# Kernel optimization log

Measured on AMD Instinct MI355X. Metric: run time of the kernel, lower is better.

Reference implementation:

```python
import jax, jax.numpy as jnp
import numpy as np
from jax import lax

H, W = 3072, 4096
BLACK = 0.0625            # black level (normalized)
KNEE_X = np.array([0.0, 0.25, 1.0], np.float32)   # decompanding curve
KNEE_Y = np.array([0.0, 0.50, 1.0], np.float32)
DEN_R, DEN_EPS = 2, 100.0         # BayerDenoise defaults
AWB_MAX_GAIN = 4.0
LTM_A, LTM_B, LTM_R, LTM_EPS = 0.7, 0.0, 8, 1e-3
GAMMA = 2.2


def _box_sum_1d(x, r, axis):
    """Sliding-window sum of width 2r+1 along `axis`, edge-truncated."""
    n = x.shape[axis]
    c = jnp.cumsum(x, axis=axis)
    hi = jnp.clip(jnp.arange(n) + r, 0, n - 1)
    lo = jnp.arange(n) - r - 1
    upper = jnp.take(c, hi, axis=axis)
    lower = jnp.take(c, jnp.clip(lo, 0, n - 1), axis=axis)
    shp = [1] * x.ndim
    shp[axis] = n
    lower = lower * (lo >= 0).astype(x.dtype).reshape(shp)
    return upper - lower


def box_mean(x, r):
    """2D box mean over last two axes, normalized by valid window counts."""
    s = _box_sum_1d(_box_sum_1d(x, r, -2), r, -1)
    cnt = _box_sum_1d(_box_sum_1d(jnp.ones_like(x), r, -2), r, -1)
    return s / cnt


def guided_self(I, r, eps):
    """Self-guided (edge-preserving) filter."""
    m = box_mean(I, r)
    var = box_mean(I * I, r) - m * m
    a = var / (var + eps)
    b = m * (1.0 - a)
    return box_mean(a, r) * I + box_mean(b, r)


def conv3x3(img, k):
    return lax.conv_general_dilated(img[None, None], k[None, None], (1, 1), 'SAME')[0, 0]


def isp_pipeline(x, ccm):
    # --- DecompandBlackLevel: piecewise-linear decompand + black level ---
    x = jnp.interp(x, jnp.asarray(KNEE_X), jnp.asarray(KNEE_Y))
    x = jnp.clip((x - BLACK) / (1.0 - BLACK), 0.0, 1.0)

    # --- BayerDenoise: guided filter on each RGGB plane ---
    p = jnp.stack([x[0::2, 0::2], x[0::2, 1::2], x[1::2, 0::2], x[1::2, 1::2]])  # [4,H/2,W/2]
    p = guided_self(p, DEN_R, DEN_EPS)

    # --- AWB: gray-world gains from plane means (lum mask [0,1] = all pixels) ---
    r_m, g_m, b_m = p[0].mean(), 0.5 * (p[1].mean() + p[2].mean()), p[3].mean()
    gr = jnp.minimum(g_m / (r_m + 1e-8), AWB_MAX_GAIN)
    gb = jnp.minimum(g_m / (b_m + 1e-8), AWB_MAX_GAIN)
    x = (jnp.zeros_like(x)
         .at[0::2, 0::2].set(jnp.clip(p[0] * gr, 0.0, 1.0))
         .at[0::2, 1::2].set(jnp.clip(p[1], 0.0, 1.0))
         .at[1::2, 0::2].set(jnp.clip(p[2], 0.0, 1.0))
         .at[1::2, 1::2].set(jnp.clip(p[3] * gb, 0.0, 1.0)))

    # --- Demosaic: bilinear on RGGB mosaic ---
    ii = (jnp.arange(H) % 2)[:, None]
    jj = (jnp.arange(W) % 2)[None, :]
    mR = ((ii == 0) & (jj == 0)).astype(x.dtype)
    mG = (ii != jj).astype(x.dtype)
    mB = ((ii == 1) & (jj == 1)).astype(x.dtype)
    k_g = jnp.array([[0, 1, 0], [1, 4, 1], [0, 1, 0]], jnp.float32) / 4.0
    k_rb = jnp.array([[1, 2, 1], [2, 4, 2], [1, 2, 1]], jnp.float32) / 4.0
    rgb = jnp.stack([conv3x3(x * mR, k_rb), conv3x3(x * mG, k_g), conv3x3(x * mB, k_rb)])  # [3,H,W]

    # --- CCM ---
    rgb = jnp.clip(jnp.einsum('ij,jhw->ihw', ccm, rgb), 0.0, 1.0)

    wl = jnp.array([0.299, 0.587, 0.114], jnp.float32)
    Y = jnp.einsum('c,chw->hw', wl, rgb)
    Ys = Y.reshape(H // 2, 2, W // 2, 2).mean(axis=(1, 3))
    base = jax.image.resize(guided_self(Ys, LTM_R, LTM_EPS), (H, W), 'bilinear')
    Ynew = LTM_A * base + LTM_B + (Y - base)       # detail_gain=1, threshold=0
    rgb = jnp.clip(rgb * (Ynew / (Y + 1e-6)), 0.0, 1.0)

    # --- Gamma ---
    rgb = jnp.clip(rgb, 1e-6, 1.0) ** (1.0 / GAMMA)
    # hist_norm / post_denoise / saturation / sharpening are identity at defaults

    # --- RGBtoYUV -> NV12 (full range BT.601) ---
    R, G, B = rgb[0], rgb[1], rgb[2]
    Yf = 0.299 * R + 0.587 * G + 0.114 * B
    U = -0.168736 * R - 0.331264 * G + 0.5 * B + 0.5
    V = 0.5 * R - 0.418688 * G - 0.081312 * B + 0.5
    Us = U.reshape(H // 2, 2, W // 2, 2).mean(axis=(1, 3))
    Vs = V.reshape(H // 2, 2, W // 2, 2).mean(axis=(1, 3))
    uv = jnp.stack([Us, Vs], axis=-1).reshape(H // 2, W)  # interleaved UVUV...
    out = jnp.concatenate([Yf.reshape(-1), uv.reshape(-1)]) * 255.0
    return jnp.clip(out, 0.0, 255.0)   # float NV12 codes (pre-quantization)


def setup_inputs() -> dict:
    key = jax.random.key(0)
    k1, k2 = jax.random.split(key)
    x = jax.random.uniform(k1, (H, W), dtype=jnp.float32)
    ccm = jnp.eye(3, dtype=jnp.float32) + 0.1 * jax.random.normal(k2, (3, 3), dtype=jnp.float32)
    return {"x": x, "ccm": ccm}


def reference(x, ccm):
    return isp_pipeline(x, ccm)
```

## Files before the change

kernel.cpp:

```cpp
#include <hip/hip_runtime.h>
#include <math.h>

#define IMG_H 3072
#define IMG_W 4096
#define Hh 1536
#define Wh 2048
#define S (Hh*Wh)

#define TID 32
#define TIL 16

#if __has_builtin(__builtin_amdgcn_rcpf)
#define RCP(x) __builtin_amdgcn_rcpf(x)
#else
#define RCP(x) (1.0f/(x))
#endif

__device__ __forceinline__ float clamp01(float v){ return fminf(fmaxf(v, 0.0f), 1.0f); }

__device__ __forceinline__ float decompand_black(float v){
  float y = (v <= 0.25f) ? (2.0f*v) : fmaf(v - 0.25f, 0.5f/0.75f, 0.5f);
  y = clamp01(y);
  return clamp01((y - 0.0625f) * (1.0f/0.9375f));
}

__device__ __forceinline__ float gamma22(float x){
  return __builtin_amdgcn_exp2f(0.45454545454545453f * __builtin_amdgcn_logf(x));
}

__global__ __launch_bounds__(256) void k_split(const float* __restrict__ x, float* __restrict__ P){
  int idx = blockIdx.x*256 + threadIdx.x;
  int i = idx >> 11, j = idx & 2047;
  const float* r0 = x + (2*i)*IMG_W + 2*j;
  const float* r1 = r0 + IMG_W;
  float2 a = *(const float2*)r0;
  float2 b = *(const float2*)r1;
  P[idx]       = decompand_black(a.x);
  P[S + idx]   = decompand_black(a.y);
  P[2*S + idx] = decompand_black(b.x);
  P[3*S + idx] = decompand_black(b.y);
}

template<int TI, bool FAST>
__device__ __forceinline__ void denoise_col(const float* __restrict__ in, float* __restrict__ D,
                                            int j, int i0, float& local){
  const float inv25 = 1.0f/25.0f;
  float cw_a[5], amask[5], cw_o = 25.f;
  if (!FAST){
    #pragma unroll
    for (int k=0;k<5;++k){
      int pc = j + k - 2;
      bool ok = ((unsigned)pc < (unsigned)Wh);
      amask[k] = ok ? 1.f : 0.f;
      cw_a[k]  = ok ? (float)(min(pc+2, Wh-1) - max(pc-2, 0) + 1) : 1.f;
    }
    cw_o = (float)(min(j+2, Wh-1) - max(j-2, 0) + 1);
  }

  float rh1[5][5]={{0}}, rh2[5][5]={{0}};
  float vs1[5]={0}, vs2[5]={0};
  float rha[5]={0}, rhb[5]={0};
  float cI[5]={0};
  float wa=0.f, wb=0.f;

  const float* rp = in + (size_t)(i0-4)*Wh + j;
  float* wp = D + (size_t)i0*Wh + j;

  #pragma unroll 4
  for (int rr=0; rr<TI+8; ++rr){
    int r = i0 - 4 + rr;
    float v[9];
    if (FAST){
      #pragma unroll
      for (int d=0; d<9; ++d) v[d] = rp[d-4];
    } else {
      if ((unsigned)r < (unsigned)Hh){
        #pragma unroll
        for (int d=0; d<9; ++d){
          int c = j + d - 4;
          v[d] = ((unsigned)c < (unsigned)Wh) ? rp[d-4] : 0.f;
        }
      } else {
        #pragma unroll
        for (int d=0; d<9; ++d) v[d]=0.f;
      }
    }
    rp += Wh;
    float sq[9];
    #pragma unroll
    for (int d=0; d<9; ++d) sq[d]=v[d]*v[d];
    float h1[5], h2[5];
    h1[0]=v[0]+v[1]+v[2]+v[3]+v[4];
    h2[0]=sq[0]+sq[1]+sq[2]+sq[3]+sq[4];
    #pragma unroll
    for (int k=1;k<5;++k){
      h1[k]=h1[k-1]-v[k-1]+v[k+4];
      h2[k]=h2[k-1]-sq[k-1]+sq[k+4];
    }
    #pragma unroll
    for (int k=0;k<5;++k){
      vs1[k]+=h1[k]-rh1[k][0];
      vs2[k]+=h2[k]-rh2[k][0];
      #pragma unroll
      for (int t=0;t<4;++t){ rh1[k][t]=rh1[k][t+1]; rh2[k][t]=rh2[k][t+1]; }
      rh1[k][4]=h1[k]; rh2[k][4]=h2[k];
    }
    #pragma unroll
    for (int t=0;t<4;++t) cI[t]=cI[t+1];
    cI[4]=v[4];

    if (rr >= 4){
      int q = r-2;
      float ha_=0.f, hb_=0.f;
      if (FAST){
        #pragma unroll
        for (int k=0;k<5;++k){
          float m   = vs1[k]*inv25;
          float var = fmaf(-m, m, vs2[k]*inv25);
          float a   = var*RCP(var + 100.0f);
          float b   = fmaf(-m, a, m);
          ha_ += a; hb_ += b;
        }
      } else {
        float rmask = ((unsigned)q < (unsigned)Hh) ? 1.f : 0.f;
        float rh = (float)(min(q+2, Hh-1) - max(q-2, 0) + 1);
        #pragma unroll
        for (int k=0;k<5;++k){
          float inv = RCP(rh*cw_a[k]);
          float m   = vs1[k]*inv;
          float var = fmaf(-m, m, vs2[k]*inv);
          float a   = var*RCP(var + 100.0f);
          float b   = fmaf(-m, a, m);
          ha_ = fmaf(a, amask[k], ha_);
          hb_ = fmaf(b, amask[k], hb_);
        }
        ha_ *= rmask; hb_ *= rmask;
      }
      wa += ha_ - rha[0];
      wb += hb_ - rhb[0];
      #pragma unroll
      for (int t=0;t<4;++t){ rha[t]=rha[t+1]; rhb[t]=rhb[t+1]; }
      rha[4]=ha_; rhb[4]=hb_;

      if (rr >= 8){
        int ro = r-4;
        float invo;
        if (FAST){
          invo = inv25;
        } else {
          float rho = (float)(min(ro+2, Hh-1) - max(ro-2, 0) + 1);
          invo = RCP(rho*cw_o);
        }
        float d = fmaf(wa*invo, cI[0], wb*invo);
        *wp = d; wp += Wh;
        local += d;
      }
    }
  }
}

template<int TI>
__global__ __launch_bounds__(256) void k_denoise(const float* __restrict__ P4,
                                                 float* __restrict__ D4,
                                                 float* __restrict__ sums){
  const int j  = blockIdx.x*256 + threadIdx.x;
  const int i0 = blockIdx.y*TI;
  const int pl = blockIdx.z;
  const float* __restrict__ in = P4 + (size_t)pl*S;
  float* __restrict__ D = D4 + (size_t)pl*S;
  float local = 0.f;

  const bool fast = (blockIdx.x >= 1) && (blockIdx.x <= (Wh/256)-2) &&
                    (blockIdx.y >= 1) && (i0 + TI + 4 <= Hh);
  if (fast) denoise_col<TI, true >(in, D, j, i0, local);
  else      denoise_col<TI, false>(in, D, j, i0, local);

  __shared__ float red[256];
  red[threadIdx.x]=local;
  __syncthreads();
  #pragma unroll
  for (int off=128; off>0; off>>=1){
    if (threadIdx.x<off) red[threadIdx.x]+=red[threadIdx.x+off];
    __syncthreads();
  }
  if (threadIdx.x==0) atomicAdd(sums+pl, red[0]);
}

template<int R, int TI>
__global__ __launch_bounds__(256) void k_boxsq_ab(const float* __restrict__ in,
                                                  float* __restrict__ A, float* __restrict__ B,
                                                  float eps){
  int j  = blockIdx.x*256 + threadIdx.x;
  int i0 = blockIdx.y*TI;
  int cw = min(j+R, Wh-1) - max(j-R, 0) + 1;

  float hs[2*R+1], hs2[2*R+1];
  float ws = 0.f, ws2 = 0.f;
  #pragma unroll
  for (int k=0; k<2*R+1; ++k){
    int r = i0 - R + k;
    float s = 0.f, s2 = 0.f;
    if ((unsigned)r < (unsigned)Hh){
      const float* row = in + r*Wh;
      #pragma unroll
      for (int d=-R; d<=R; ++d){
        int c = j + d;
        float v = ((unsigned)c < (unsigned)Wh) ? row[c] : 0.f;
        s += v; s2 = fmaf(v, v, s2);
      }
    }
    hs[k] = s; hs2[k] = s2; ws += s; ws2 += s2;
  }
  #pragma unroll
  for (int t=0; t<TI; ++t){
    int i = i0 + t;
    int rh = min(i+R, Hh-1) - max(i-R, 0) + 1;
    float inv = 1.0f/(float)(rh*cw);
    float m   = ws*inv;
    float var = fmaf(-m, m, ws2*inv);
    float a   = var/(var + eps);
    A[i*Wh + j] = a;
    B[i*Wh + j] = m*(1.0f - a);
    if (t < TI-1){
      ws -= hs[0]; ws2 -= hs2[0];
      #pragma unroll
      for (int k=0; k<2*R; ++k){ hs[k]=hs[k+1]; hs2[k]=hs2[k+1]; }
      int r = i + R + 1;
      float s = 0.f, s2 = 0.f;
      if (r < Hh){
        const float* row = in + r*Wh;
        #pragma unroll
        for (int d=-R; d<=R; ++d){
          int c = j + d;
          float v = ((unsigned)c < (unsigned)Wh) ? row[c] : 0.f;
          s += v; s2 = fmaf(v, v, s2);
        }
      }
      hs[2*R] = s; hs2[2*R] = s2; ws += s; ws2 += s2;
    }
  }
}

template<int R, int TI>
__global__ __launch_bounds__(256) void k_box_apply(const float* __restrict__ in,
                                                   const float* __restrict__ A, const float* __restrict__ B,
                                                   float* __restrict__ D){
  int j  = blockIdx.x*256 + threadIdx.x;
  int i0 = blockIdx.y*TI;
  int cw = min(j+R, Wh-1) - max(j-R, 0) + 1;

  float ha[2*R+1], hb[2*R+1];
  float wa = 0.f, wb = 0.f;
  #pragma unroll
  for (int k=0; k<2*R+1; ++k){
    int r = i0 - R + k;
    float sa = 0.f, sb = 0.f;
    if ((unsigned)r < (unsigned)Hh){
      const float* ra = A + r*Wh;
      const float* rb = B + r*Wh;
      #pragma unroll
      for (int d=-R; d<=R; ++d){
        int c = j + d;
        bool ok = ((unsigned)c < (unsigned)Wh);
        sa += ok ? ra[c] : 0.f;
        sb += ok ? rb[c] : 0.f;
      }
    }
    ha[k] = sa; hb[k] = sb; wa += sa; wb += sb;
  }
  #pragma unroll
  for (int t=0; t<TI; ++t){
    int i = i0 + t;
    int rh = min(i+R, Hh-1) - max(i-R, 0) + 1;
    float inv = 1.0f/(float)(rh*cw);
    D[i*Wh + j] = fmaf(wa*inv, in[i*Wh + j], wb*inv);
    if (t < TI-1){
      wa -= ha[0]; wb -= hb[0];
      #pragma unroll
      for (int k=0; k<2*R; ++k){ ha[k]=ha[k+1]; hb[k]=hb[k+1]; }
      int r = i + R + 1;
      float sa = 0.f, sb = 0.f;
      if (r < Hh){
        const float* ra = A + r*Wh;
        const float* rb = B + r*Wh;
        #pragma unroll
        for (int d2=-R; d2<=R; ++d2){
          int c = j + d2;
          bool ok = ((unsigned)c < (unsigned)Wh);
          sa += ok ? ra[c] : 0.f;
          sb += ok ? rb[c] : 0.f;
        }
      }
      ha[2*R] = sa; hb[2*R] = sb; wa += sa; wb += sb;
    }
  }
}

__global__ void k_gains(const float* __restrict__ sums, float* __restrict__ gains){
  if (threadIdx.x == 0 && blockIdx.x == 0){
    const float inv = 1.0f/(float)S;
    float rm = sums[0]*inv, g1 = sums[1]*inv, g2 = sums[2]*inv, bm = sums[3]*inv;
    float gm = 0.5f*(g1+g2);
    gains[0] = fminf(gm/(rm + 1e-8f), 4.0f);
    gains[1] = fminf(gm/(bm + 1e-8f), 4.0f);
  }
}

__device__ __forceinline__ void load_mosaic(const float* __restrict__ D, float gr, float gb,
                                            int i, int j, float m[4][4]){
  const float* __restrict__ P0 = D;
  const float* __restrict__ P1 = D + (size_t)S;
  const float* __restrict__ P2 = D + (size_t)2*S;
  const float* __restrict__ P3 = D + (size_t)3*S;
  const bool up = (i > 0), dn = (i < Hh-1), lf = (j > 0), rt = (j < Wh-1);
  const size_t rc = (size_t)i*Wh + j;
  const size_t ru = rc - Wh, rd = rc + Wh;
  m[0][0] = (up && lf) ? clamp01(P3[ru-1]*gb) : 0.f;
  m[0][1] = up ? clamp01(P2[ru]) : 0.f;
  m[0][2] = up ? clamp01(P3[ru]*gb) : 0.f;
  m[0][3] = (up && rt) ? clamp01(P2[ru+1]) : 0.f;
  m[1][0] = lf ? clamp01(P1[rc-1]) : 0.f;
  m[1][1] = clamp01(P0[rc]*gr);
  m[1][2] = clamp01(P1[rc]);
  m[1][3] = rt ? clamp01(P0[rc+1]*gr) : 0.f;
  m[2][0] = lf ? clamp01(P3[rc-1]*gb) : 0.f;
  m[2][1] = clamp01(P2[rc]);
  m[2][2] = clamp01(P3[rc]*gb);
  m[2][3] = rt ? clamp01(P2[rc+1]) : 0.f;
  m[3][0] = (dn && lf) ? clamp01(P1[rd-1]) : 0.f;
  m[3][1] = dn ? clamp01(P0[rd]*gr) : 0.f;
  m[3][2] = dn ? clamp01(P1[rd]) : 0.f;
  m[3][3] = (dn && rt) ? clamp01(P0[rd+1]*gr) : 0.f;
}

__device__ __forceinline__ void demosaic_ccm(const float m[4][4], const float* __restrict__ C,
                                             float R[2][2], float G[2][2], float Bv[2][2]){
  float r[2][2], g[2][2], b[2][2];
  r[0][0] = m[1][1];
  g[0][0] = 0.25f*(m[0][1]+m[2][1]+m[1][0]+m[1][2]);
  b[0][0] = 0.25f*(m[0][0]+m[0][2]+m[2][0]+m[2][2]);
  r[0][1] = 0.5f*(m[1][1]+m[1][3]);
  g[0][1] = m[1][2];
  b[0][1] = 0.5f*(m[0][2]+m[2][2]);
  r[1][0] = 0.5f*(m[1][1]+m[3][1]);
  g[1][0] = m[2][1];
  b[1][0] = 0.5f*(m[2][0]+m[2][2]);
  r[1][1] = 0.25f*(m[1][1]+m[1][3]+m[3][1]+m[3][3]);
  g[1][1] = 0.25f*(m[1][2]+m[3][2]+m[2][1]+m[2][3]);
  b[1][1] = m[2][2];
  #pragma unroll
  for (int a=0; a<2; ++a){
    #pragma unroll
    for (int c=0; c<2; ++c){
      R[a][c]  = clamp01(fmaf(C[2], b[a][c], fmaf(C[1], g[a][c], C[0]*r[a][c])));
      G[a][c]  = clamp01(fmaf(C[5], b[a][c], fmaf(C[4], g[a][c], C[3]*r[a][c])));
      Bv[a][c] = clamp01(fmaf(C[8], b[a][c], fmaf(C[7], g[a][c], C[6]*r[a][c])));
    }
  }
}

__global__ __launch_bounds__(256) void k_ys(const float* __restrict__ D, const float* __restrict__ gains,
                                            const float* __restrict__ C, float* __restrict__ Ys){
  int idx = blockIdx.x*256 + threadIdx.x;
  int i = idx >> 11, j = idx & 2047;
  float gr = gains[0], gb = gains[1];
  float m[4][4]; load_mosaic(D, gr, gb, i, j, m);
  float R[2][2], G[2][2], Bv[2][2];
  demosaic_ccm(m, C, R, G, Bv);
  float y = 0.f;
  #pragma unroll
  for (int a=0; a<2; ++a)
    #pragma unroll
    for (int c=0; c<2; ++c)
      y += 0.299f*R[a][c] + 0.587f*G[a][c] + 0.114f*Bv[a][c];
  Ys[idx] = 0.25f*y;
}

__global__ __launch_bounds__(256) void k_final(const float* __restrict__ D, const float* __restrict__ gains,
                                               const float* __restrict__ C,
                                               const float* __restrict__ bs, float* __restrict__ out){
  int idx = blockIdx.x*256 + threadIdx.x;
  int i = idx >> 11, j = idx & 2047;
  float gr = gains[0], gb = gains[1];
  float m[4][4]; load_mosaic(D, gr, gb, i, j, m);
  float R[2][2], G[2][2], Bv[2][2];
  demosaic_ccm(m, C, R, G, Bv);

  float bsv[3][3];
  #pragma unroll
  for (int a=0; a<3; ++a){
    int r = min(max(i-1+a, 0), Hh-1);
    #pragma unroll
    for (int b=0; b<3; ++b){
      int c = min(max(j-1+b, 0), Wh-1);
      bsv[a][b] = bs[(r<<11) + c];
    }
  }
  float base[2][2];
  base[0][0] = 0.0625f*bsv[0][0] + 0.1875f*bsv[0][1] + 0.1875f*bsv[1][0] + 0.5625f*bsv[1][1];
  base[0][1] = 0.1875f*bsv[0][1] + 0.0625f*bsv[0][2] + 0.5625f*bsv[1][1] + 0.1875f*bsv[1][2];
  base[1][0] = 0.1875f*bsv[1][0] + 0.5625f*bsv[1][1] + 0.0625f*bsv[2][0] + 0.1875f*bsv[2][1];
  base[1][1] = 0.5625f*bsv[1][1] + 0.1875f*bsv[1][2] + 0.1875f*bsv[2][1] + 0.0625f*bsv[2][2];

  float Yp[2][2];
  float Uacc = 0.f, Vacc = 0.f;
  #pragma unroll
  for (int a=0; a<2; ++a){
    #pragma unroll
    for (int c=0; c<2; ++c){
      float Yl   = 0.299f*R[a][c] + 0.587f*G[a][c] + 0.114f*Bv[a][c];
      float Ynew = fmaf(0.7f, base[a][c], Yl - base[a][c]);
      float sc   = Ynew/(Yl + 1e-6f);
      float Rg = gamma22(fmaxf(clamp01(R[a][c]*sc),  1e-6f));
      float Gg = gamma22(fmaxf(clamp01(G[a][c]*sc),  1e-6f));
      float Bg = gamma22(fmaxf(clamp01(Bv[a][c]*sc), 1e-6f));
      float Yf = 0.299f*Rg + 0.587f*Gg + 0.114f*Bg;
      Yp[a][c] = fminf(fmaxf(Yf*255.0f, 0.0f), 255.0f);
      Uacc += -0.168736f*Rg - 0.331264f*Gg + 0.5f*Bg + 0.5f;
      Vacc +=  0.5f*Rg - 0.418688f*Gg - 0.081312f*Bg + 0.5f;
    }
  }
  *(float2*)(out + (2*i)*IMG_W   + 2*j) = make_float2(Yp[0][0], Yp[0][1]);
  *(float2*)(out + (2*i+1)*IMG_W + 2*j) = make_float2(Yp[1][0], Yp[1][1]);
  float u = fminf(fmaxf(0.25f*Uacc*255.0f, 0.0f), 255.0f);
  float v = fminf(fmaxf(0.25f*Vacc*255.0f, 0.0f), 255.0f);
  *(float2*)(out + IMG_H*IMG_W + i*IMG_W + 2*j) = make_float2(u, v);
}

extern "C" void kernel_launch(void* const* d_in, const int* in_sizes, int n_in,
                              void* d_out, int out_size, void* d_ws, size_t ws_size,
                              hipStream_t stream){
  const float* x   = (const float*)d_in[0];
  const float* ccm = (const float*)d_in[1];
  float* ws  = (float*)d_ws;
  float* out = (float*)d_out;

  size_t need = ((size_t)10*S + 8)*sizeof(float);
  if (ws_size < need) return;

  float* P  = ws;
  float* D  = ws + (size_t)4*S;
  float* Ys = ws + (size_t)8*S;
  float* La = ws + (size_t)9*S;
  float* Lb = ws;
  float* bs = ws + (size_t)S;
  float* sums  = ws + (size_t)10*S;
  float* gains = sums + 4;

  const int nb = S/256;
  dim3 gdn(Wh/256, Hh/TID, 4);
  dim3 gltm(Wh/256, Hh/TIL);

  k_split<<<nb, 256, 0, stream>>>(x, P);
  (void)hipMemsetAsync(sums, 0, 4*sizeof(float), stream);
  k_denoise<TID><<<gdn, 256, 0, stream>>>(P, D, sums);
  k_gains<<<1, 64, 0, stream>>>(sums, gains);
  k_ys<<<nb, 256, 0, stream>>>(D, gains, ccm, Ys);
  k_boxsq_ab<8, TIL><<<gltm, 256, 0, stream>>>(Ys, La, Lb, 1e-3f);
  k_box_apply<8, TIL><<<gltm, 256, 0, stream>>>(Ys, La, Lb, bs);
  k_final<<<nb, 256, 0, stream>>>(D, gains, ccm, bs, out);
}
```

Baseline: 329.8 us.

## Process two columns per thread in split, denoise, ys and final kernels

Each thread now handles two adjacent half-res columns, so horizontal box sums and neighbor loads are shared between outputs, and loads and stores are vectorized as float2 and float4. The memset and the separate gains kernel are dropped: sums are zeroed inside k_split and gains are computed inline from sums in consumers. The aim is fewer memory transactions and fewer launches, at the cost of higher register pressure in denoise and half as many threads.

```diff
diff --git a/kernel.cpp b/kernel.cpp
--- a/kernel.cpp
+++ b/kernel.cpp
@@ -28,77 +28,85 @@
   return __builtin_amdgcn_exp2f(0.45454545454545453f * __builtin_amdgcn_logf(x));
 }
 
-__global__ __launch_bounds__(256) void k_split(const float* __restrict__ x, float* __restrict__ P){
+__global__ __launch_bounds__(256) void k_split(const float* __restrict__ x, float* __restrict__ P,
+                                               float* __restrict__ sums){
   int idx = blockIdx.x*256 + threadIdx.x;
-  int i = idx >> 11, j = idx & 2047;
-  const float* r0 = x + (2*i)*IMG_W + 2*j;
-  const float* r1 = r0 + IMG_W;
-  float2 a = *(const float2*)r0;
-  float2 b = *(const float2*)r1;
-  P[idx]       = decompand_black(a.x);
-  P[S + idx]   = decompand_black(a.y);
-  P[2*S + idx] = decompand_black(b.x);
-  P[3*S + idx] = decompand_black(b.y);
+  int i = idx >> 10, jq = (idx & 1023)*2;
+  const float* r0 = x + (size_t)(2*i)*IMG_W + 2*jq;
+  float4 a = *(const float4*)r0;
+  float4 b = *(const float4*)(r0 + IMG_W);
+  size_t o = (size_t)i*Wh + jq;
+  *(float2*)(P + o)            = make_float2(decompand_black(a.x), decompand_black(a.z));
+  *(float2*)(P + S + o)        = make_float2(decompand_black(a.y), decompand_black(a.w));
+  *(float2*)(P + 2*(size_t)S + o) = make_float2(decompand_black(b.x), decompand_black(b.z));
+  *(float2*)(P + 3*(size_t)S + o) = make_float2(decompand_black(b.y), decompand_black(b.w));
+  if (blockIdx.x == 0 && threadIdx.x < 4) sums[threadIdx.x] = 0.f;
 }
 
 template<int TI, bool FAST>
-__device__ __forceinline__ void denoise_col(const float* __restrict__ in, float* __restrict__ D,
-                                            int j, int i0, float& local){
+__device__ __forceinline__ void denoise_col2(const float* __restrict__ in, float* __restrict__ D,
+                                             int c0, int i0, float& local){
   const float inv25 = 1.0f/25.0f;
-  float cw_a[5], amask[5], cw_o = 25.f;
+  float cw_a[6], amask[6], cw_o0 = 25.f, cw_o1 = 25.f;
   if (!FAST){
     #pragma unroll
-    for (int k=0;k<5;++k){
-      int pc = j + k - 2;
+    for (int k=0;k<6;++k){
+      int pc = c0 + k - 2;
       bool ok = ((unsigned)pc < (unsigned)Wh);
       amask[k] = ok ? 1.f : 0.f;
       cw_a[k]  = ok ? (float)(min(pc+2, Wh-1) - max(pc-2, 0) + 1) : 1.f;
     }
-    cw_o = (float)(min(j+2, Wh-1) - max(j-2, 0) + 1);
-  }
-
-  float rh1[5][5]={{0}}, rh2[5][5]={{0}};
-  float vs1[5]={0}, vs2[5]={0};
-  float rha[5]={0}, rhb[5]={0};
-  float cI[5]={0};
-  float wa=0.f, wb=0.f;
-
-  const float* rp = in + (size_t)(i0-4)*Wh + j;
-  float* wp = D + (size_t)i0*Wh + j;
+    cw_o0 = (float)(min(c0+2, Wh-1)   - max(c0-2, 0) + 1);
+    cw_o1 = (float)(min(c0+3, Wh-1)   - max(c0-1, 0) + 1);
+  }
+
+  float rh1[6][5]={{0}}, rh2[6][5]={{0}};
+  float vs1[6]={0}, vs2[6]={0};
+  float rha0[5]={0}, rhb0[5]={0}, rha1[5]={0}, rhb1[5]={0};
+  float cI0[5]={0}, cI1[5]={0};
+  float wa0=0.f, wb0=0.f, wa1=0.f, wb1=0.f;
+
+  const float* rp = in + (size_t)(i0-4)*Wh + c0;
+  float* wp = D + (size_t)i0*Wh + c0;
 
   #pragma unroll 4
   for (int rr=0; rr<TI+8; ++rr){
     int r = i0 - 4 + rr;
-    float v[9];
+    float v[10];
     if (FAST){
-      #pragma unroll
-      for (int d=0; d<9; ++d) v[d] = rp[d-4];
+      float2 p0 = *(const float2*)(rp-4);
+      float2 p1 = *(const float2*)(rp-2);
+      float2 p2 = *(const float2*)(rp);
+      float2 p3 = *(const float2*)(rp+2);
+      float2 p4 = *(const float2*)(rp+4);
+      v[0]=p0.x; v[1]=p0.y; v[2]=p1.x; v[3]=p1.y; v[4]=p2.x;
+      v[5]=p2.y; v[6]=p3.x; v[7]=p3.y; v[8]=p4.x; v[9]=p4.y;
     } else {
       if ((unsigned)r < (unsigned)Hh){
         #pragma unroll
-        for (int d=0; d<9; ++d){
-          int c = j + d - 4;
+        for (int d=0; d<10; ++d){
+          int c = c0 + d - 4;
           v[d] = ((unsigned)c < (unsigned)Wh) ? rp[d-4] : 0.f;
         }
       } else {
         #pragma unroll
-        for (int d=0; d<9; ++d) v[d]=0.f;
+        for (int d=0; d<10; ++d) v[d]=0.f;
       }
     }
     rp += Wh;
-    float sq[9];
-    #pragma unroll
-    for (int d=0; d<9; ++d) sq[d]=v[d]*v[d];
-    float h1[5], h2[5];
+    float sq[10];
+    #pragma unroll
+    for (int d=0; d<10; ++d) sq[d]=v[d]*v[d];
+    float h1[6], h2[6];
     h1[0]=v[0]+v[1]+v[2]+v[3]+v[4];
     h2[0]=sq[0]+sq[1]+sq[2]+sq[3]+sq[4];
     #pragma unroll
-    for (int k=1;k<5;++k){
+    for (int k=1;k<6;++k){
       h1[k]=h1[k-1]-v[k-1]+v[k+4];
       h2[k]=h2[k-1]-sq[k-1]+sq[k+4];
     }
     #pragma unroll
-    for (int k=0;k<5;++k){
+    for (int k=0;k<6;++k){
       vs1[k]+=h1[k]-rh1[k][0];
       vs2[k]+=h2[k]-rh2[k][0];
       #pragma unroll
@@ -106,54 +114,58 @@
       rh1[k][4]=h1[k]; rh2[k][4]=h2[k];
     }
     #pragma unroll
-    for (int t=0;t<4;++t) cI[t]=cI[t+1];
-    cI[4]=v[4];
+    for (int t=0;t<4;++t){ cI0[t]=cI0[t+1]; cI1[t]=cI1[t+1]; }
+    cI0[4]=v[4]; cI1[4]=v[5];
 
     if (rr >= 4){
       int q = r-2;
-      float ha_=0.f, hb_=0.f;
+      float a6[6], b6[6];
       if (FAST){
         #pragma unroll
-        for (int k=0;k<5;++k){
+        for (int k=0;k<6;++k){
           float m   = vs1[k]*inv25;
           float var = fmaf(-m, m, vs2[k]*inv25);
           float a   = var*RCP(var + 100.0f);
-          float b   = fmaf(-m, a, m);
-          ha_ += a; hb_ += b;
+          a6[k] = a; b6[k] = fmaf(-m, a, m);
         }
       } else {
         float rmask = ((unsigned)q < (unsigned)Hh) ? 1.f : 0.f;
         float rh = (float)(min(q+2, Hh-1) - max(q-2, 0) + 1);
         #pragma unroll
-        for (int k=0;k<5;++k){
+        for (int k=0;k<6;++k){
           float inv = RCP(rh*cw_a[k]);
           float m   = vs1[k]*inv;
           float var = fmaf(-m, m, vs2[k]*inv);
           float a   = var*RCP(var + 100.0f);
           float b   = fmaf(-m, a, m);
-          ha_ = fmaf(a, amask[k], ha_);
-          hb_ = fmaf(b, amask[k], hb_);
+          a6[k] = a*amask[k]*rmask; b6[k] = b*amask[k]*rmask;
         }
-        ha_ *= rmask; hb_ *= rmask;
-      }
-      wa += ha_ - rha[0];
-      wb += hb_ - rhb[0];
-      #pragma unroll
-      for (int t=0;t<4;++t){ rha[t]=rha[t+1]; rhb[t]=rhb[t+1]; }
-      rha[4]=ha_; rhb[4]=hb_;
+      }
+      float ha0 = a6[0]+a6[1]+a6[2]+a6[3]+a6[4];
+      float hb0 = b6[0]+b6[1]+b6[2]+b6[3]+b6[4];
+      float ha1 = ha0 - a6[0] + a6[5];
+      float hb1 = hb0 - b6[0] + b6[5];
+      wa0 += ha0 - rha0[0]; wb0 += hb0 - rhb0[0];
+      wa1 += ha1 - rha1[0]; wb1 += hb1 - rhb1[0];
+      #pragma unroll
+      for (int t=0;t<4;++t){
+        rha0[t]=rha0[t+1]; rhb0[t]=rhb0[t+1];
+        rha1[t]=rha1[t+1]; rhb1[t]=rhb1[t+1];
+      }
+      rha0[4]=ha0; rhb0[4]=hb0; rha1[4]=ha1; rhb1[4]=hb1;
 
       if (rr >= 8){
         int ro = r-4;
-        float invo;
-        if (FAST){
-          invo = inv25;
-        } else {
+        float invo0, invo1;
+        if (FAST){ invo0 = inv25; invo1 = inv25; }
+        else {
           float rho = (float)(min(ro+2, Hh-1) - max(ro-2, 0) + 1);
-          invo = RCP(rho*cw_o);
+          invo0 = RCP(rho*cw_o0); invo1 = RCP(rho*cw_o1);
         }
-        float d = fmaf(wa*invo, cI[0], wb*invo);
-        *wp = d; wp += Wh;
-        local += d;
+        float d0 = fmaf(wa0*invo0, cI0[0], wb0*invo0);
+        float d1 = fmaf(wa1*invo1, cI1[0], wb1*invo1);
+        *(float2*)wp = make_float2(d0, d1); wp += Wh;
+        local += d0 + d1;
       }
     }
   }
@@ -163,17 +175,18 @@
 __global__ __launch_bounds__(256) void k_denoise(const float* __restrict__ P4,
                                                  float* __restrict__ D4,
                                                  float* __restrict__ sums){
-  const int j  = blockIdx.x*256 + threadIdx.x;
+  const int c0 = (blockIdx.x*256 + threadIdx.x)*2;
   const int i0 = blockIdx.y*TI;
   const int pl = blockIdx.z;
   const float* __restrict__ in = P4 + (size_t)pl*S;
   float* __restrict__ D = D4 + (size_t)pl*S;
   float local = 0.f;
 
-  const bool fast = (blockIdx.x >= 1) && (blockIdx.x <= (Wh/256)-2) &&
-                    (blockIdx.y >= 1) && (i0 + TI + 4 <= Hh);
-  if (fast) denoise_col<TI, true >(in, D, j, i0, local);
-  else      denoise_col<TI, false>(in, D, j, i0, local);
+  const int cmin = (blockIdx.x*256 + (threadIdx.x & ~63))*2;
+  const bool rows_ok = (i0 >= 4) && (i0 + TI + 4 <= Hh);
+  const bool fast = rows_ok && (cmin >= 4) && (cmin + 131 < Wh);
+  if (fast) denoise_col2<TI, true >(in, D, c0, i0, local);
+  else      denoise_col2<TI, false>(in, D, c0, i0, local);
 
   __shared__ float red[256];
   red[threadIdx.x]=local;
@@ -296,58 +309,84 @@
   }
 }
 
-__global__ void k_gains(const float* __restrict__ sums, float* __restrict__ gains){
-  if (threadIdx.x == 0 && blockIdx.x == 0){
-    const float inv = 1.0f/(float)S;
-    float rm = sums[0]*inv, g1 = sums[1]*inv, g2 = sums[2]*inv, bm = sums[3]*inv;
-    float gm = 0.5f*(g1+g2);
-    gains[0] = fminf(gm/(rm + 1e-8f), 4.0f);
-    gains[1] = fminf(gm/(bm + 1e-8f), 4.0f);
-  }
-}
-
-__device__ __forceinline__ void load_mosaic(const float* __restrict__ D, float gr, float gb,
-                                            int i, int j, float m[4][4]){
+__device__ __forceinline__ void awb_gains(const float* __restrict__ sums, float& gr, float& gb){
+  const float invS = 1.0f/(float)S;
+  float rm = sums[0]*invS, g1 = sums[1]*invS, g2 = sums[2]*invS, bm = sums[3]*invS;
+  float gm = 0.5f*(g1+g2);
+  gr = fminf(gm/(rm + 1e-8f), 4.0f);
+  gb = fminf(gm/(bm + 1e-8f), 4.0f);
+}
+
+__device__ __forceinline__ void load_mosaic2(const float* __restrict__ D, float gr, float gb,
+                                             int i, int j, float m[4][6]){
   const float* __restrict__ P0 = D;
   const float* __restrict__ P1 = D + (size_t)S;
   const float* __restrict__ P2 = D + (size_t)2*S;
   const float* __restrict__ P3 = D + (size_t)3*S;
-  const bool up = (i > 0), dn = (i < Hh-1), lf = (j > 0), rt = (j < Wh-1);
+  const bool up = (i > 0), dn = (i < Hh-1), lf = (j > 0), rt = (j+2 < Wh);
   const size_t rc = (size_t)i*Wh + j;
   const size_t ru = rc - Wh, rd = rc + Wh;
-  m[0][0] = (up && lf) ? clamp01(P3[ru-1]*gb) : 0.f;
-  m[0][1] = up ? clamp01(P2[ru]) : 0.f;
-  m[0][2] = up ? clamp01(P3[ru]*gb) : 0.f;
-  m[0][3] = (up && rt) ? clamp01(P2[ru+1]) : 0.f;
-  m[1][0] = lf ? clamp01(P1[rc-1]) : 0.f;
-  m[1][1] = clamp01(P0[rc]*gr);
-  m[1][2] = clamp01(P1[rc]);
-  m[1][3] = rt ? clamp01(P0[rc+1]*gr) : 0.f;
-  m[2][0] = lf ? clamp01(P3[rc-1]*gb) : 0.f;
-  m[2][1] = clamp01(P2[rc]);
-  m[2][2] = clamp01(P3[rc]*gb);
-  m[2][3] = rt ? clamp01(P2[rc+1]) : 0.f;
-  m[3][0] = (dn && lf) ? clamp01(P1[rd-1]) : 0.f;
-  m[3][1] = dn ? clamp01(P0[rd]*gr) : 0.f;
-  m[3][2] = dn ? clamp01(P1[rd]) : 0.f;
-  m[3][3] = (dn && rt) ? clamp01(P0[rd+1]*gr) : 0.f;
-}
-
-__device__ __forceinline__ void demosaic_ccm(const float m[4][4], const float* __restrict__ C,
-                                             float R[2][2], float G[2][2], float Bv[2][2]){
+  const float2 z = make_float2(0.f, 0.f);
+  {
+    float2 t3 = up ? *(const float2*)(P3+ru) : z;
+    float2 t2 = up ? *(const float2*)(P2+ru) : z;
+    m[0][0] = (up&&lf) ? clamp01(P3[ru-1]*gb) : 0.f;
+    m[0][1] = clamp01(t2.x);
+    m[0][2] = clamp01(t3.x*gb);
+    m[0][3] = clamp01(t2.y);
+    m[0][4] = clamp01(t3.y*gb);
+    m[0][5] = (up&&rt) ? clamp01(P2[ru+2]) : 0.f;
+  }
+  {
+    float2 t1 = *(const float2*)(P1+rc);
+    float2 t0 = *(const float2*)(P0+rc);
+    m[1][0] = lf ? clamp01(P1[rc-1]) : 0.f;
+    m[1][1] = clamp01(t0.x*gr);
+    m[1][2] = clamp01(t1.x);
+    m[1][3] = clamp01(t0.y*gr);
+    m[1][4] = clamp01(t1.y);
+    m[1][5] = rt ? clamp01(P0[rc+2]*gr) : 0.f;
+  }
+  {
+    float2 s3 = *(const float2*)(P3+rc);
+    float2 s2 = *(const float2*)(P2+rc);
+    m[2][0] = lf ? clamp01(P3[rc-1]*gb) : 0.f;
+    m[2][1] = clamp01(s2.x);
+    m[2][2] = clamp01(s3.x*gb);
+    m[2][3] = clamp01(s2.y);
+    m[2][4] = clamp01(s3.y*gb);
+    m[2][5] = rt ? clamp01(P2[rc+2]) : 0.f;
+  }
+  {
+    float2 u1 = dn ? *(const float2*)(P1+rd) : z;
+    float2 u0 = dn ? *(const float2*)(P0+rd) : z;
+    m[3][0] = (dn&&lf) ? clamp01(P1[rd-1]) : 0.f;
+    m[3][1] = clamp01(u0.x*gr);
+    m[3][2] = clamp01(u1.x);
+    m[3][3] = clamp01(u0.y*gr);
+    m[3][4] = clamp01(u1.y);
+    m[3][5] = (dn&&rt) ? clamp01(P0[rd+2]*gr) : 0.f;
+  }
+}
+
+template<int O>
+__device__ __forceinline__ void demosaic_ccm_s(const float m[4][6], const float* __restrict__ C,
+                                               float R[2][2], float G[2][2], float Bv[2][2]){
+  #define MM(a,b) m[a][(b)+2*O]
   float r[2][2], g[2][2], b[2][2];
-  r[0][0] = m[1][1];
-  g[0][0] = 0.25f*(m[0][1]+m[2][1]+m[1][0]+m[1][2]);
-  b[0][0] = 0.25f*(m[0][0]+m[0][2]+m[2][0]+m[2][2]);
-  r[0][1] = 0.5f*(m[1][1]+m[1][3]);
-  g[0][1] = m[1][2];
-  b[0][1] = 0.5f*(m[0][2]+m[2][2]);
-  r[1][0] = 0.5f*(m[1][1]+m[3][1]);
-  g[1][0] = m[2][1];
-  b[1][0] = 0.5f*(m[2][0]+m[2][2]);
-  r[1][1] = 0.25f*(m[1][1]+m[1][3]+m[3][1]+m[3][3]);
-  g[1][1] = 0.25f*(m[1][2]+m[3][2]+m[2][1]+m[2][3]);
-  b[1][1] = m[2][2];
+  r[0][0] = MM(1,1);
+  g[0][0] = 0.25f*(MM(0,1)+MM(2,1)+MM(1,0)+MM(1,2));
+  b[0][0] = 0.25f*(MM(0,0)+MM(0,2)+MM(2,0)+MM(2,2));
+  r[0][1] = 0.5f*(MM(1,1)+MM(1,3));
+  g[0][1] = MM(1,2);
+  b[0][1] = 0.5f*(MM(0,2)+MM(2,2));
+  r[1][0] = 0.5f*(MM(1,1)+MM(3,1));
+  g[1][0] = MM(2,1);
+  b[1][0] = 0.5f*(MM(2,0)+MM(2,2));
+  r[1][1] = 0.25f*(MM(1,1)+MM(1,3)+MM(3,1)+MM(3,3));
+  g[1][1] = 0.25f*(MM(1,2)+MM(3,2)+MM(2,1)+MM(2,3));
+  b[1][1] = MM(2,2);
+  #undef MM
   #pragma unroll
   for (int a=0; a<2; ++a){
     #pragma unroll
@@ -359,72 +398,89 @@
   }
 }
 
-__global__ __launch_bounds__(256) void k_ys(const float* __restrict__ D, const float* __restrict__ gains,
+__global__ __launch_bounds__(256) void k_ys(const float* __restrict__ D, const float* __restrict__ sums,
                                             const float* __restrict__ C, float* __restrict__ Ys){
   int idx = blockIdx.x*256 + threadIdx.x;
-  int i = idx >> 11, j = idx & 2047;
-  float gr = gains[0], gb = gains[1];
-  float m[4][4]; load_mosaic(D, gr, gb, i, j, m);
-  float R[2][2], G[2][2], Bv[2][2];
-  demosaic_ccm(m, C, R, G, Bv);
-  float y = 0.f;
-  #pragma unroll
-  for (int a=0; a<2; ++a)
-    #pragma unroll
-    for (int c=0; c<2; ++c)
-      y += 0.299f*R[a][c] + 0.587f*G[a][c] + 0.114f*Bv[a][c];
-  Ys[idx] = 0.25f*y;
-}
-
-__global__ __launch_bounds__(256) void k_final(const float* __restrict__ D, const float* __restrict__ gains,
+  int i = idx >> 10, j = (idx & 1023)*2;
+  float gr, gb; awb_gains(sums, gr, gb);
+  float m[4][6]; load_mosaic2(D, gr, gb, i, j, m);
+  float y0 = 0.f, y1 = 0.f;
+  {
+    float R[2][2], G[2][2], Bv[2][2];
+    demosaic_ccm_s<0>(m, C, R, G, Bv);
+    #pragma unroll
+    for (int a=0; a<2; ++a)
+      #pragma unroll
+      for (int c=0; c<2; ++c)
+        y0 += 0.299f*R[a][c] + 0.587f*G[a][c] + 0.114f*Bv[a][c];
+  }
+  {
+    float R[2][2], G[2][2], Bv[2][2];
+    demosaic_ccm_s<1>(m, C, R, G, Bv);
+    #pragma unroll
+    for (int a=0; a<2; ++a)
+      #pragma unroll
+      for (int c=0; c<2; ++c)
+        y1 += 0.299f*R[a][c] + 0.587f*G[a][c] + 0.114f*Bv[a][c];
+  }
+  *(float2*)(Ys + (size_t)i*Wh + j) = make_float2(0.25f*y0, 0.25f*y1);
+}
+
+__global__ __launch_bounds__(256) void k_final(const float* __restrict__ D, const float* __restrict__ sums,
                                                const float* __restrict__ C,
                                                const float* __restrict__ bs, float* __restrict__ out){
   int idx = blockIdx.x*256 + threadIdx.x;
-  int i = idx >> 11, j = idx & 2047;
-  float gr = gains[0], gb = gains[1];
-  float m[4][4]; load_mosaic(D, gr, gb, i, j, m);
-  float R[2][2], G[2][2], Bv[2][2];
-  demosaic_ccm(m, C, R, G, Bv);
-
-  float bsv[3][3];
+  int i = idx >> 10, j = (idx & 1023)*2;
+  float gr, gb; awb_gains(sums, gr, gb);
+  float m[4][6]; load_mosaic2(D, gr, gb, i, j, m);
+
+  float bsv[3][4];
   #pragma unroll
   for (int a=0; a<3; ++a){
     int r = min(max(i-1+a, 0), Hh-1);
-    #pragma unroll
-    for (int b=0; b<3; ++b){
-      int c = min(max(j-1+b, 0), Wh-1);
-      bsv[a][b] = bs[(r<<11) + c];
-    }
-  }
-  float base[2][2];
-  base[0][0] = 0.0625f*bsv[0][0] + 0.1875f*bsv[0][1] + 0.1875f*bsv[1][0] + 0.5625f*bsv[1][1];
-  base[0][1] = 0.1875f*bsv[0][1] + 0.0625f*bsv[0][2] + 0.5625f*bsv[1][1] + 0.1875f*bsv[1][2];
-  base[1][0] = 0.1875f*bsv[1][0] + 0.5625f*bsv[1][1] + 0.0625f*bsv[2][0] + 0.1875f*bsv[2][1];
-  base[1][1] = 0.5625f*bsv[1][1] + 0.1875f*bsv[1][2] + 0.1875f*bsv[2][1] + 0.0625f*bsv[2][2];
-
-  float Yp[2][2];
-  float Uacc = 0.f, Vacc = 0.f;
-  #pragma unroll
-  for (int a=0; a<2; ++a){
-    #pragma unroll
-    for (int c=0; c<2; ++c){
-      float Yl   = 0.299f*R[a][c] + 0.587f*G[a][c] + 0.114f*Bv[a][c];
-      float Ynew = fmaf(0.7f, base[a][c], Yl - base[a][c]);
-      float sc   = Ynew/(Yl + 1e-6f);
-      float Rg = gamma22(fmaxf(clamp01(R[a][c]*sc),  1e-6f));
-      float Gg = gamma22(fmaxf(clamp01(G[a][c]*sc),  1e-6f));
-      float Bg = gamma22(fmaxf(clamp01(Bv[a][c]*sc), 1e-6f));
-      float Yf = 0.299f*Rg + 0.587f*Gg + 0.114f*Bg;
-      Yp[a][c] = fminf(fmaxf(Yf*255.0f, 0.0f), 255.0f);
-      Uacc += -0.168736f*Rg - 0.331264f*Gg + 0.5f*Bg + 0.5f;
-      Vacc +=  0.5f*Rg - 0.418688f*Gg - 0.081312f*Bg + 0.5f;
-    }
-  }
-  *(float2*)(out + (2*i)*IMG_W   + 2*j) = make_float2(Yp[0][0], Yp[0][1]);
-  *(float2*)(out + (2*i+1)*IMG_W + 2*j) = make_float2(Yp[1][0], Yp[1][1]);
-  float u = fminf(fmaxf(0.25f*Uacc*255.0f, 0.0f), 255.0f);
-  float v = fminf(fmaxf(0.25f*Vacc*255.0f, 0.0f), 255.0f);
-  *(float2*)(out + IMG_H*IMG_W + i*IMG_W + 2*j) = make_float2(u, v);
+    const float* br = bs + ((size_t)r<<11);
+    bsv[a][0] = br[max(j-1, 0)];
+    float2 t = *(const float2*)(br + j);
+    bsv[a][1] = t.x; bsv[a][2] = t.y;
+    bsv[a][3] = br[min(j+2, Wh-1)];
+  }
+
+  float Yrow0[4], Yrow1[4], UV[4];
+  #pragma unroll
+  for (int o=0; o<2; ++o){
+    float R[2][2], G[2][2], Bv[2][2];
+    if (o==0) demosaic_ccm_s<0>(m, C, R, G, Bv);
+    else      demosaic_ccm_s<1>(m, C, R, G, Bv);
+    float base[2][2];
+    base[0][0] = 0.0625f*bsv[0][0+o] + 0.1875f*bsv[0][1+o] + 0.1875f*bsv[1][0+o] + 0.5625f*bsv[1][1+o];
+    base[0][1] = 0.1875f*bsv[0][1+o] + 0.0625f*bsv[0][2+o] + 0.5625f*bsv[1][1+o] + 0.1875f*bsv[1][2+o];
+    base[1][0] = 0.1875f*bsv[1][0+o] + 0.5625f*bsv[1][1+o] + 0.0625f*bsv[2][0+o] + 0.1875f*bsv[2][1+o];
+    base[1][1] = 0.5625f*bsv[1][1+o] + 0.1875f*bsv[1][2+o] + 0.1875f*bsv[2][1+o] + 0.0625f*bsv[2][2+o];
+
+    float Uacc = 0.f, Vacc = 0.f;
+    #pragma unroll
+    for (int a=0; a<2; ++a){
+      #pragma unroll
+      for (int c=0; c<2; ++c){
+        float Yl   = 0.299f*R[a][c] + 0.587f*G[a][c] + 0.114f*Bv[a][c];
+        float Ynew = fmaf(0.7f, base[a][c], Yl - base[a][c]);
+        float sc   = Ynew/(Yl + 1e-6f);
+        float Rg = gamma22(fmaxf(clamp01(R[a][c]*sc),  1e-6f));
+        float Gg = gamma22(fmaxf(clamp01(G[a][c]*sc),  1e-6f));
+        float Bg = gamma22(fmaxf(clamp01(Bv[a][c]*sc), 1e-6f));
+        float Yf = 0.299f*Rg + 0.587f*Gg + 0.114f*Bg;
+        float Yq = fminf(fmaxf(Yf*255.0f, 0.0f), 255.0f);
+        if (a==0) Yrow0[2*o+c] = Yq; else Yrow1[2*o+c] = Yq;
+        Uacc += -0.168736f*Rg - 0.331264f*Gg + 0.5f*Bg + 0.5f;
+        Vacc +=  0.5f*Rg - 0.418688f*Gg - 0.081312f*Bg + 0.5f;
+      }
+    }
+    UV[2*o]   = fminf(fmaxf(0.25f*Uacc*255.0f, 0.0f), 255.0f);
+    UV[2*o+1] = fminf(fmaxf(0.25f*Vacc*255.0f, 0.0f), 255.0f);
+  }
+  *(float4*)(out + (size_t)(2*i)*IMG_W   + 2*j) = make_float4(Yrow0[0], Yrow0[1], Yrow0[2], Yrow0[3]);
+  *(float4*)(out + (size_t)(2*i+1)*IMG_W + 2*j) = make_float4(Yrow1[0], Yrow1[1], Yrow1[2], Yrow1[3]);
+  *(float4*)(out + (size_t)IMG_H*IMG_W + (size_t)i*IMG_W + 2*j) = make_float4(UV[0], UV[1], UV[2], UV[3]);
 }
 
 extern "C" void kernel_launch(void* const* d_in, const int* in_sizes, int n_in,
@@ -445,18 +501,15 @@
   float* Lb = ws;
   float* bs = ws + (size_t)S;
   float* sums  = ws + (size_t)10*S;
-  float* gains = sums + 4;
-
-  const int nb = S/256;
-  dim3 gdn(Wh/256, Hh/TID, 4);
+
+  const int nb2 = S/512;
+  dim3 gdn(Wh/512, Hh/TID, 4);
   dim3 gltm(Wh/256, Hh/TIL);
 
-  k_split<<<nb, 256, 0, stream>>>(x, P);
-  (void)hipMemsetAsync(sums, 0, 4*sizeof(float), stream);
+  k_split<<<nb2, 256, 0, stream>>>(x, P, sums);
   k_denoise<TID><<<gdn, 256, 0, stream>>>(P, D, sums);
-  k_gains<<<1, 64, 0, stream>>>(sums, gains);
-  k_ys<<<nb, 256, 0, stream>>>(D, gains, ccm, Ys);
+  k_ys<<<nb2, 256, 0, stream>>>(D, sums, ccm, Ys);
   k_boxsq_ab<8, TIL><<<gltm, 256, 0, stream>>>(Ys, La, Lb, 1e-3f);
   k_box_apply<8, TIL><<<gltm, 256, 0, stream>>>(Ys, La, Lb, bs);
-  k_final<<<nb, 256, 0, stream>>>(D, gains, ccm, bs, out);
-}
+  k_final<<<nb2, 256, 0, stream>>>(D, sums, ccm, bs, out);
+}
```

Result: faster. 320.4 us (-2.9%).
